# Kernel optimization log

Hardware: AMD Instinct MI355X
Metric: run time of the kernel (lower is better)

## Reference

```python
import jax, jax.numpy as jnp
import numpy as np

EPS = 1e-5
K = 20

def lrelu(x):
    return jnp.where(x >= 0, x, 0.2 * x)

def in2d(x):  # [B,C,N,k] instance norm over (N,k), no affine, biased var
    m = jnp.mean(x, axis=(2, 3), keepdims=True)
    v = jnp.var(x, axis=(2, 3), keepdims=True)
    return (x - m) * jax.lax.rsqrt(v + EPS)

def in1d(x):  # [B,C,N] instance norm over N
    m = jnp.mean(x, axis=2, keepdims=True)
    v = jnp.var(x, axis=2, keepdims=True)
    return (x - m) * jax.lax.rsqrt(v + EPS)

def knn_idx(x, k):  # x: [B,C,N]; uses only first 3 channels (as original)
    p = x[:, :3, :]
    inner = -2.0 * jnp.einsum('bcn,bcm->bnm', p, p)
    xx = jnp.sum(p * p, axis=1)  # [B,N]
    pd = -xx[:, :, None] - inner - xx[:, None, :]  # negative squared dist [B,N,N]
    return jax.lax.top_k(pd, k)[1]  # [B,N,k]

def graph_feature(x, k):  # x: [B,C,N] -> [B,2C,N,k]
    idx = knn_idx(x, k)
    xT = jnp.transpose(x, (0, 2, 1))  # [B,N,C]
    feat = jax.vmap(lambda t, i: t[i])(xT, idx)  # [B,N,k,C]
    center = xT[:, :, None, :]
    out = jnp.concatenate([feat - center, jnp.broadcast_to(center, feat.shape)], axis=3)
    return jnp.transpose(out, (0, 3, 1, 2))  # [B,2C,N,k]

def conv2d1(w, x):  # 1x1 conv2d: w [O,C], x [B,C,N,k]
    return jnp.einsum('oc,bcnk->bonk', w, x)

def conv1d1(w, x):  # 1x1 conv1d: w [O,C], x [B,C,N]
    return jnp.einsum('oc,bcn->bon', w, x)

def setup_inputs() -> dict:
    key = jax.random.key(0)
    ks = jax.random.split(key, 10)
    def w(k, o, c):
        return jax.random.normal(k, (o, c), dtype=jnp.float32) * np.float32(1.0 / np.sqrt(c))
    return {
        'x':  jax.random.normal(ks[0], (4, 4096, 4), dtype=jnp.float32),
        'w1': w(ks[1], 64, 8),
        'w2': w(ks[2], 64, 64),
        'w3': w(ks[3], 64, 128),
        'w4': w(ks[4], 64, 64),
        'w5': w(ks[5], 64, 128),
        'w6': w(ks[6], 1024, 192),
        'w7': w(ks[7], 512, 1216),
        'w8': w(ks[8], 256, 512),
        'w9': w(ks[9], 2, 256),
    }

def reference(x, w1, w2, w3, w4, w5, w6, w7, w8, w9):
    xt = jnp.transpose(x, (0, 2, 1))  # [B,4,N]
    num_points = xt.shape[2]
    # EdgeConv block 1
    f = graph_feature(xt, K)                     # [B,8,N,k]
    h = lrelu(in2d(conv2d1(w1, f)))
    h = lrelu(in2d(conv2d1(w2, h)))
    x1 = jnp.max(h, axis=-1)                     # [B,64,N]
    # EdgeConv block 2
    f = graph_feature(x1, K)                     # [B,128,N,k]
    h = lrelu(in2d(conv2d1(w3, f)))
    h = lrelu(in2d(conv2d1(w4, h)))
    x2 = jnp.max(h, axis=-1)
    # EdgeConv block 3
    f = graph_feature(x2, K)
    h = lrelu(in2d(conv2d1(w5, f)))
    x3 = jnp.max(h, axis=-1)
    # global embedding
    cat = jnp.concatenate([x1, x2, x3], axis=1)  # [B,192,N]
    g = lrelu(in1d(conv1d1(w6, cat)))            # [B,1024,N]
    g = jnp.max(g, axis=-1, keepdims=True)       # [B,1024,1]
    g = jnp.broadcast_to(g, (g.shape[0], g.shape[1], num_points))
    h = jnp.concatenate([g, x1, x2, x3], axis=1) # [B,1216,N]
    h = lrelu(in1d(conv1d1(w7, h)))
    h = lrelu(in1d(conv1d1(w8, h)))
    # dropout identity (eval mode)
    out = conv1d1(w9, h)                         # [B,2,N]
    return jnp.transpose(out, (0, 2, 1))         # [B,N,2]
```

## Files before the change

kernel.cpp:

```cpp
#include <hip/hip_runtime.h>
#include <hip/hip_fp16.h>
#include <math.h>

constexpr int BB  = 4;
constexpr int NN  = 4096;
constexpr int KK  = 20;
constexpr int NKK = NN * KK;
constexpr int TPOS = BB * NKK;
constexpr int NMASK = NN - 1;

#define DEVFN __device__ __forceinline__

DEVFN float lrelu_f(float v) { return v >= 0.f ? v : 0.2f * v; }
DEVFN unsigned fenc(float f) { unsigned u = __float_as_uint(f); return (u & 0x80000000u) ? ~u : (u | 0x80000000u); }

template<int CSTRIDE>
__global__ __launch_bounds__(256) void knn_kernel(const float* __restrict__ xin, int* __restrict__ idxout)
{
    __shared__ float sx[NN], sy[NN], sz[NN];
    __shared__ unsigned shist[256];
    __shared__ unsigned scollv[256];
    __shared__ unsigned long long scoll64[128];
    __shared__ unsigned sres[2];
    __shared__ unsigned scnt[2];
    const int tid = threadIdx.x;
    const int b  = blockIdx.x >> 8;
    const int q0 = (blockIdx.x & 255) * 16;
    for (int i = tid; i < NN; i += 256) {
        const float4 rc = *reinterpret_cast<const float4*>(xin + (size_t)(b*NN + i) * CSTRIDE);
        sx[i] = rc.x; sy[i] = rc.y; sz[i] = rc.z;
    }

    for (int qq = 0; qq < 16; ++qq) {
        __syncthreads();
        shist[tid] = 0;
        if (tid == 0) { scnt[0] = 0; scnt[1] = 0; }
        const int qi = q0 + qq;
        const float qx = sx[qi], qy = sy[qi], qz = sz[qi];
        const float nxx = -__fadd_rn(__fadd_rn(__fmul_rn(qx,qx), __fmul_rn(qy,qy)), __fmul_rn(qz,qz));
        __syncthreads();
        unsigned ukey[NN/256];
#pragma unroll
        for (int i = 0; i < NN/256; ++i) {
            const int m = tid + (i << 8);
            float cx = sx[m], cy = sy[m], cz = sz[m];
            float cw  = __fadd_rn(__fadd_rn(__fmul_rn(cx,cx), __fmul_rn(cy,cy)), __fmul_rn(cz,cz));
            float dot = __fadd_rn(__fadd_rn(__fmul_rn(qx,cx), __fmul_rn(qy,cy)), __fmul_rn(qz,cz));
            float pd  = __fsub_rn(__fsub_rn(nxx, __fmul_rn(-2.f, dot)), cw);
            unsigned u = fenc(pd);
            ukey[i] = u;
            atomicAdd(&shist[u >> 24], 1u);
        }
        __syncthreads();
        if (tid < 64) {
            const int base = 255 - tid*4;
            unsigned h0 = shist[base], h1 = shist[base-1], h2 = shist[base-2], h3 = shist[base-3];
            unsigned s = h0 + h1 + h2 + h3;
            unsigned c = s;
#pragma unroll
            for (int off = 1; off < 64; off <<= 1) { unsigned t = __shfl_up(c, off, 64); if (tid >= off) c += t; }
            unsigned cprev = c - s;
            if (c >= KK && cprev < KK) {
                unsigned cc = cprev; int bb = base;
                if (cc + h0 < KK) { cc += h0; bb = base-1;
                    if (cc + h1 < KK) { cc += h1; bb = base-2;
                        if (cc + h2 < KK) { cc += h2; bb = base-3; } } }
                sres[0] = (unsigned)bb; sres[1] = KK - cc;
            }
        }
        __syncthreads();
        const unsigned b0 = sres[0], K1 = sres[1];
        shist[tid] = 0;
        __syncthreads();
#pragma unroll
        for (int i = 0; i < NN/256; ++i) {
            unsigned u = ukey[i];
            if ((u >> 24) == b0) atomicAdd(&shist[(u >> 16) & 255u], 1u);
        }
        __syncthreads();
        if (tid < 64) {
            const int base = 255 - tid*4;
            unsigned h0 = shist[base], h1 = shist[base-1], h2 = shist[base-2], h3 = shist[base-3];
            unsigned s = h0 + h1 + h2 + h3;
            unsigned c = s;
#pragma unroll
            for (int off = 1; off < 64; off <<= 1) { unsigned t = __shfl_up(c, off, 64); if (tid >= off) c += t; }
            unsigned cprev = c - s;
            if (c >= K1 && cprev < K1) {
                unsigned cc = cprev; int bb = base;
                if (cc + h0 < K1) { cc += h0; bb = base-1;
                    if (cc + h1 < K1) { cc += h1; bb = base-2;
                        if (cc + h2 < K1) { cc += h2; bb = base-3; } } }
                sres[0] = (unsigned)bb; sres[1] = K1 - cc;
            }
        }
        __syncthreads();
        const unsigned prefix16 = (b0 << 8) | sres[0];
        const unsigned K2 = sres[1];
#pragma unroll
        for (int i = 0; i < NN/256; ++i) {
            unsigned u = ukey[i];
            if ((u >> 16) == prefix16) {
                unsigned pos = atomicAdd(&scnt[0], 1u);
                if (pos < 256u) scollv[pos] = u;
            }
        }
        __syncthreads();
        {
            int cb = (int)scnt[0]; if (cb > 256) cb = 256;
            if (tid < cb) {
                unsigned v = scollv[tid];
                unsigned ng = 0, ne = 0;
                for (int j = 0; j < cb; ++j) {
                    unsigned w = scollv[j];
                    ng += (w > v); ne += (w == v);
                }
                if (ng < K2 && ng + ne >= K2) sres[0] = v;
            }
        }
        __syncthreads();
        const unsigned W = sres[0];
#pragma unroll
        for (int i = 0; i < NN/256; ++i) {
            const int m = tid + (i << 8);
            unsigned u = ukey[i];
            if (u >= W) {
                unsigned pos = atomicAdd(&scnt[1], 1u);
                if (pos < 128u) scoll64[pos] = ((unsigned long long)u << 32) | (unsigned)(NN-1 - m);
            }
        }
        __syncthreads();
        {
            int c2 = (int)scnt[1]; if (c2 > 128) c2 = 128;
            if (tid < c2) {
                unsigned long long kv = scoll64[tid];
                int rank = 0;
                for (int j = 0; j < c2; ++j) rank += (scoll64[j] > kv);
                if (rank < KK) {
                    int* op = idxout + ((size_t)(b*NN + qi)) * KK;
                    op[rank] = (NN-1) - (int)(kv & 0xFFFFFFFFull);
                }
            }
        }
    }
}

template<int CINH, int CSTRIDE>
__global__ __launch_bounds__(64) void uv_kernel(const float* __restrict__ xin, const float* __restrict__ w,
                                                float* __restrict__ ub, float* __restrict__ vb)
{
    __shared__ float sp[32][CINH];
    const int lane = threadIdx.x;
    float wa[CINH], wd[CINH];
#pragma unroll
    for (int c = 0; c < CINH; ++c) {
        float a = w[lane*(2*CINH) + c];
        wa[c] = a;
        wd[c] = w[lane*(2*CINH) + CINH + c] - a;
    }
    const int p0 = blockIdx.x * 32;
    for (int i = lane; i < 32*CINH; i += 64) {
        int pi = i / CINH, c = i % CINH;
        sp[pi][c] = xin[(size_t)(p0 + pi)*CSTRIDE + c];
    }
    __syncthreads();
    for (int pi = 0; pi < 32; ++pi) {
        float au = 0.f, av = 0.f;
#pragma unroll
        for (int c = 0; c < CINH; ++c) {
            float xv = sp[pi][c];
            au = fmaf(wa[c], xv, au);
            av = fmaf(wd[c], xv, av);
        }
        ub[(size_t)(p0 + pi)*64 + lane] = au;
        vb[(size_t)(p0 + pi)*64 + lane] = av;
    }
}

template<bool STOREMAX>
__global__ __launch_bounds__(64) void gstat_kernel(const float* __restrict__ ub, const float* __restrict__ vb,
    const int* __restrict__ idx, float* __restrict__ xraw,
    double* __restrict__ ssum, double* __restrict__ ssq)
{
    const int lane = threadIdx.x;
    const int g0 = blockIdx.x * 8;
    const int b = g0 / NN;
    double lsum = 0.0, lsq = 0.0;
    for (int ni = 0; ni < 8; ++ni) {
        const int g = g0 + ni;
        const float v = vb[(size_t)g*64 + lane];
        float vmax = -INFINITY;
        for (int k = 0; k < KK; ++k) {
            const int j = idx[(size_t)g*KK + k] & NMASK;
            float o = ub[(size_t)(b*NN + j)*64 + lane] + v;
            if constexpr (STOREMAX) vmax = fmaxf(vmax, o);
            lsum += (double)o; lsq += (double)o*(double)o;
        }
        if constexpr (STOREMAX) xraw[(size_t)g*64 + lane] = vmax;
    }
    atomicAdd(&ssum[b*64+lane], lsum);
    atomicAdd(&ssq [b*64+lane], lsq);
}

__global__ __launch_bounds__(64) void s1b_kernel(const float* __restrict__ x, const int* __restrict__ idx,
    const float* __restrict__ w1, const float* __restrict__ w2,
    const float* __restrict__ m1, const float* __restrict__ r1,
    float* __restrict__ xraw, double* __restrict__ ssum, double* __restrict__ ssq)
{
    __shared__ float sh[64];
    const int lane = threadIdx.x;
    float wr1[8];
#pragma unroll
    for (int c = 0; c < 8; ++c) wr1[c] = w1[lane*8 + c];
    float wr2[64];
#pragma unroll
    for (int c = 0; c < 64; ++c) wr2[c] = w2[lane*64 + c];
    const int g0 = blockIdx.x * 8;
    const int b = g0 / NN;
    const float mm = m1[b*64+lane], rr = r1[b*64+lane];
    double lsum = 0.0, lsq = 0.0;
    for (int ni = 0; ni < 8; ++ni) {
        const int g = g0 + ni;
        const float4 ct = *reinterpret_cast<const float4*>(x + (size_t)g*4);
        float vmax = -INFINITY;
        for (int k = 0; k < KK; ++k) {
            const int j = idx[(size_t)g*KK + k] & NMASK;
            const float4 nb = *reinterpret_cast<const float4*>(x + (size_t)(b*NN + j)*4);
            float o1 = wr1[0]*(nb.x-ct.x) + wr1[1]*(nb.y-ct.y) + wr1[2]*(nb.z-ct.z) + wr1[3]*(nb.w-ct.w)
                     + wr1[4]*ct.x + wr1[5]*ct.y + wr1[6]*ct.z + wr1[7]*ct.w;
            float h = lrelu_f((o1 - mm) * rr);
            __syncthreads();
            sh[lane] = h;
            __syncthreads();
            float acc = 0.f;
#pragma unroll
            for (int c = 0; c < 64; c += 4) {
                const float4 hv = *reinterpret_cast<const float4*>(&sh[c]);
                acc += wr2[c]*hv.x + wr2[c+1]*hv.y + wr2[c+2]*hv.z + wr2[c+3]*hv.w;
            }
            vmax = fmaxf(vmax, acc);
            lsum += (double)acc; lsq += (double)acc*(double)acc;
        }
        xraw[(size_t)g*64 + lane] = vmax;
    }
    atomicAdd(&ssum[b*64+lane], lsum);
    atomicAdd(&ssq [b*64+lane], lsq);
}

__global__ __launch_bounds__(64) void s2b_kernel(const float* __restrict__ xin, const int* __restrict__ idx,
    const float* __restrict__ w3, const float* __restrict__ w4,
    const float* __restrict__ m3, const float* __restrict__ r3,
    float* __restrict__ xraw, double* __restrict__ ssum, double* __restrict__ ssq)
{
    __shared__ float sf[128];
    __shared__ float sh[64];
    const int lane = threadIdx.x;
    float wr3[128];
#pragma unroll
    for (int c = 0; c < 128; ++c) wr3[c] = w3[lane*128 + c];
    float wr4[64];
#pragma unroll
    for (int c = 0; c < 64; ++c) wr4[c] = w4[lane*64 + c];
    const int g0 = blockIdx.x * 8;
    const int b = g0 / NN;
    const float mm = m3[b*64+lane], rr = r3[b*64+lane];
    double lsum = 0.0, lsq = 0.0;
    for (int ni = 0; ni < 8; ++ni) {
        const int g = g0 + ni;
        const float ctl = xin[(size_t)g*64 + lane];
        float vmax = -INFINITY;
        for (int k = 0; k < KK; ++k) {
            const int j = idx[(size_t)g*KK + k] & NMASK;
            const float nbl = xin[(size_t)(b*NN + j)*64 + lane];
            __syncthreads();
            sf[lane] = nbl - ctl;
            sf[64+lane] = ctl;
            __syncthreads();
            float o3 = 0.f;
#pragma unroll
            for (int c = 0; c < 128; c += 4) {
                const float4 fv = *reinterpret_cast<const float4*>(&sf[c]);
                o3 += wr3[c]*fv.x + wr3[c+1]*fv.y + wr3[c+2]*fv.z + wr3[c+3]*fv.w;
            }
            float h = lrelu_f((o3 - mm) * rr);
            __syncthreads();
            sh[lane] = h;
            __syncthreads();
            float acc = 0.f;
#pragma unroll
            for (int c = 0; c < 64; c += 4) {
                const float4 hv = *reinterpret_cast<const float4*>(&sh[c]);
                acc += wr4[c]*hv.x + wr4[c+1]*hv.y + wr4[c+2]*hv.z + wr4[c+3]*hv.w;
            }
            vmax = fmaxf(vmax, acc);
            lsum += (double)acc; lsq += (double)acc*(double)acc;
        }
        xraw[(size_t)g*64 + lane] = vmax;
    }
    atomicAdd(&ssum[b*64+lane], lsum);
    atomicAdd(&ssq [b*64+lane], lsq);
}

__global__ void fin_kernel(const double* __restrict__ ssum, const double* __restrict__ ssq,
                           float* __restrict__ meanp, float* __restrict__ rstdp, int total, double invn)
{
    int t = blockIdx.x*256 + threadIdx.x;
    if (t >= total) return;
    double m = ssum[t]*invn;
    double v = ssq[t]*invn - m*m;
    meanp[t] = (float)m;
    rstdp[t] = (float)(1.0 / sqrt(v + 1e-5));
}

__global__ void finx_kernel(float* __restrict__ xv, const float* __restrict__ m, const float* __restrict__ r)
{
    int t = blockIdx.x*256 + threadIdx.x;
    int c0 = (t & 15) * 4;
    int b = t >> 16;
    float4 v = *reinterpret_cast<float4*>(xv + (size_t)t*4);
    v.x = lrelu_f((v.x - m[b*64+c0+0]) * r[b*64+c0+0]);
    v.y = lrelu_f((v.y - m[b*64+c0+1]) * r[b*64+c0+1]);
    v.z = lrelu_f((v.z - m[b*64+c0+2]) * r[b*64+c0+2]);
    v.w = lrelu_f((v.w - m[b*64+c0+3]) * r[b*64+c0+3]);
    *reinterpret_cast<float4*>(xv + (size_t)t*4) = v;
}

__global__ void transw_kernel(const float* __restrict__ w, float* __restrict__ wT, int O, int C, int rs, int off)
{
    int t = blockIdx.x*256 + threadIdx.x;
    if (t >= O*C) return;
    int o = t % O, c = t / O;
    wT[t] = w[(size_t)o*rs + off + c];
}

__global__ __launch_bounds__(256) void conv7a_kernel(
    const float* __restrict__ x1, const float* __restrict__ x2, const float* __restrict__ x3,
    const float* __restrict__ wT,
    __half* __restrict__ out7h, double* __restrict__ ssum, double* __restrict__ ssq)
{
    __shared__ float si[32][192];
    const int b = blockIdx.z, nbase = blockIdx.x*32;
    const int o = blockIdx.y*256 + threadIdx.x;
    for (int i = threadIdx.x; i < 32*192; i += 256) {
        int nl = i/192, c = i%192;
        size_t base = (size_t)(b*NN + nbase + nl)*64;
        si[nl][c] = (c < 64) ? x1[base + c] : (c < 128) ? x2[base + c - 64] : x3[base + c - 128];
    }
    __syncthreads();
    float acc[32];
#pragma unroll
    for (int n = 0; n < 32; ++n) acc[n] = 0.f;
    for (int c = 0; c < 192; ++c) {
        float wv = wT[(size_t)c*512 + o];
#pragma unroll
        for (int n = 0; n < 32; ++n) acc[n] = fmaf(wv, si[n][c], acc[n]);
    }
    double ps = 0.0, pq = 0.0;
#pragma unroll
    for (int n = 0; n < 32; ++n) {
        out7h[(size_t)(b*NN + nbase + n)*512 + o] = __float2half(acc[n]);
        ps += (double)acc[n]; pq += (double)acc[n]*(double)acc[n];
    }
    atomicAdd(&ssum[b*512+o], ps);
    atomicAdd(&ssq [b*512+o], pq);
}

__global__ __launch_bounds__(256) void conv8k_kernel(
    const __half* __restrict__ out7h, const float* __restrict__ m7, const float* __restrict__ r7,
    const float* __restrict__ wT8,
    float* __restrict__ out8, double* __restrict__ ssum, double* __restrict__ ssq)
{
    __shared__ float h7[16][512];
    const int b = blockIdx.y, nbase = blockIdx.x*16;
    const int tid = threadIdx.x;
    for (int i = tid; i < 16*512; i += 256) {
        int nl = i >> 9, c = i & 511;
        float v = __half2float(out7h[(size_t)(b*NN + nbase + nl)*512 + c]);
        h7[nl][c] = lrelu_f((v - m7[b*512+c]) * r7[b*512+c]);
    }
    __syncthreads();
    const int o = tid;
    float acc8[16];
#pragma unroll
    for (int n = 0; n < 16; ++n) acc8[n] = 0.f;
    for (int c = 0; c < 512; ++c) {
        float wv = wT8[(size_t)c*256 + o];
#pragma unroll
        for (int n = 0; n < 16; ++n) acc8[n] = fmaf(wv, h7[n][c], acc8[n]);
    }
    double ps = 0.0, pq = 0.0;
#pragma unroll
    for (int n = 0; n < 16; ++n) {
        out8[(size_t)(b*NN + nbase + n)*256 + o] = acc8[n];
        ps += (double)acc8[n]; pq += (double)acc8[n]*(double)acc8[n];
    }
    atomicAdd(&ssum[b*256+o], ps);
    atomicAdd(&ssq [b*256+o], pq);
}

__global__ __launch_bounds__(256) void conv9_kernel(const float* __restrict__ in8,
    const float* __restrict__ meanp, const float* __restrict__ rstdp,
    const float* __restrict__ w9, float* __restrict__ outp)
{
    const int lane = threadIdx.x & 63, wv = threadIdx.x >> 6;
    const int ng = blockIdx.x*4 + wv;
    const int b = ng / NN;
    const int c0 = lane*4;
    const float4 v4 = *reinterpret_cast<const float4*>(&in8[(size_t)ng*256 + c0]);
    float vv[4] = {v4.x, v4.y, v4.z, v4.w};
    float a0 = 0.f, a1 = 0.f;
#pragma unroll
    for (int i = 0; i < 4; ++i) {
        int c = c0 + i;
        float a = lrelu_f((vv[i] - meanp[b*256+c]) * rstdp[b*256+c]);
        a0 = fmaf(w9[c],     a, a0);
        a1 = fmaf(w9[256+c], a, a1);
    }
#pragma unroll
    for (int off = 32; off > 0; off >>= 1) {
        a0 += __shfl_down(a0, off, 64);
        a1 += __shfl_down(a1, off, 64);
    }
    if (lane == 0) { outp[(size_t)ng*2 + 0] = a0; outp[(size_t)ng*2 + 1] = a1; }
}

extern "C" void kernel_launch(void* const* d_in, const int* in_sizes, int n_in,
                              void* d_out, int out_size, void* d_ws, size_t ws_size,
                              hipStream_t stream)
{
    const float* x  = (const float*)d_in[0];
    const float* w1 = (const float*)d_in[1];
    const float* w2 = (const float*)d_in[2];
    const float* w3 = (const float*)d_in[3];
    const float* w4 = (const float*)d_in[4];
    const float* w5 = (const float*)d_in[5];
    const float* w7 = (const float*)d_in[7];
    const float* w8 = (const float*)d_in[8];
    const float* w9 = (const float*)d_in[9];
    float* outp = (float*)d_out;

    char* ws = (char*)d_ws;
    size_t off = 0;
    auto alloc = [&](size_t bytes) -> void* {
        void* p = ws + off;
        off = (off + bytes + 255) & ~(size_t)255;
        return p;
    };
    double* dstats = (double*)alloc((size_t)16896 * 8);
    unsigned* u6max = (unsigned*)alloc((size_t)4096 * 4);
    float* fstats = (float*)alloc((size_t)14848 * 4);
    int*   idxb  = (int*)  alloc((size_t)TPOS * 4);
    float* wT7   = (float*)alloc((size_t)512*192*4);
    float* wT8   = (float*)alloc((size_t)256*512*4);
    char*  sc17  = (char*) alloc((size_t)BB*NN*512*2);
    float* ubuf  = (float*)sc17;
    float* vbuf  = (float*)(sc17 + (size_t)BB*NN*64*4);
    __half* out7h = (__half*)sc17;
    float* x1v   = (float*)alloc((size_t)BB*NN*64*4);
    float* x2v   = (float*)alloc((size_t)BB*NN*64*4);
    float* x3v   = (float*)alloc((size_t)BB*NN*64*4);
    float* out8  = (float*)alloc((size_t)BB*NN*256*4);

    (void)u6max;
    double* d1 = dstats;           double* d2 = dstats + 512;
    double* d3 = dstats + 1024;    double* d4 = dstats + 1536;
    double* d5 = dstats + 2048;
    double* d7sum = dstats + 10752; double* d7sq = d7sum + 2048;
    double* d8sum = dstats + 14848; double* d8sq = d8sum + 1024;
    float* m1 = fstats;        float* r1 = fstats + 256;
    float* m2 = fstats + 512;  float* r2 = fstats + 768;
    float* m3 = fstats + 1024; float* r3 = fstats + 1280;
    float* m4 = fstats + 1536; float* r4 = fstats + 1792;
    float* m5 = fstats + 2048; float* r5 = fstats + 2304;
    float* m7 = fstats + 6656; float* r7 = fstats + 8704;
    float* m8 = fstats + 12800; float* r8 = fstats + 13824;

    hipMemsetAsync(dstats, 0, (size_t)16896*8 + (size_t)4096*4, stream);

    transw_kernel<<<384, 256, 0, stream>>>(w7, wT7, 512, 192, 1216, 1024);
    transw_kernel<<<512, 256, 0, stream>>>(w8, wT8, 256, 512, 512, 0);

    knn_kernel<4><<<1024, 256, 0, stream>>>(x, idxb);
    uv_kernel<4, 4><<<512, 64, 0, stream>>>(x, w1, ubuf, vbuf);
    gstat_kernel<false><<<2048, 64, 0, stream>>>(ubuf, vbuf, idxb, nullptr, d1, d1+256);
    fin_kernel<<<1, 256, 0, stream>>>(d1, d1+256, m1, r1, 256, 1.0/81920.0);
    s1b_kernel<<<2048, 64, 0, stream>>>(x, idxb, w1, w2, m1, r1, x1v, d2, d2+256);
    fin_kernel<<<1, 256, 0, stream>>>(d2, d2+256, m2, r2, 256, 1.0/81920.0);
    finx_kernel<<<1024, 256, 0, stream>>>(x1v, m2, r2);

    knn_kernel<64><<<1024, 256, 0, stream>>>(x1v, idxb);
    uv_kernel<64, 64><<<512, 64, 0, stream>>>(x1v, w3, ubuf, vbuf);
    gstat_kernel<false><<<2048, 64, 0, stream>>>(ubuf, vbuf, idxb, nullptr, d3, d3+256);
    fin_kernel<<<1, 256, 0, stream>>>(d3, d3+256, m3, r3, 256, 1.0/81920.0);
    s2b_kernel<<<2048, 64, 0, stream>>>(x1v, idxb, w3, w4, m3, r3, x2v, d4, d4+256);
    fin_kernel<<<1, 256, 0, stream>>>(d4, d4+256, m4, r4, 256, 1.0/81920.0);
    finx_kernel<<<1024, 256, 0, stream>>>(x2v, m4, r4);

    knn_kernel<64><<<1024, 256, 0, stream>>>(x2v, idxb);
    uv_kernel<64, 64><<<512, 64, 0, stream>>>(x2v, w5, ubuf, vbuf);
    gstat_kernel<true><<<2048, 64, 0, stream>>>(ubuf, vbuf, idxb, x3v, d5, d5+256);
    fin_kernel<<<1, 256, 0, stream>>>(d5, d5+256, m5, r5, 256, 1.0/81920.0);
    finx_kernel<<<1024, 256, 0, stream>>>(x3v, m5, r5);

    conv7a_kernel<<<dim3(128, 2, 4), 256, 0, stream>>>(x1v, x2v, x3v, wT7, out7h, d7sum, d7sq);
    fin_kernel<<<8, 256, 0, stream>>>(d7sum, d7sq, m7, r7, 2048, 1.0/4096.0);
    conv8k_kernel<<<dim3(256, 4), 256, 0, stream>>>(out7h, m7, r7, wT8, out8, d8sum, d8sq);
    fin_kernel<<<4, 256, 0, stream>>>(d8sum, d8sq, m8, r8, 1024, 1.0/4096.0);
    conv9_kernel<<<4096, 256, 0, stream>>>(out8, m8, r8, w9, outp);
}
```

Baseline: 1.559 ms.

## Process two kNN queries per block concurrently and widen gstat to one point per wave

```diff
diff --git a/kernel.cpp b/kernel.cpp
--- a/kernel.cpp
+++ b/kernel.cpp
@@ -18,12 +18,13 @@
 __global__ __launch_bounds__(256) void knn_kernel(const float* __restrict__ xin, int* __restrict__ idxout)
 {
     __shared__ float sx[NN], sy[NN], sz[NN];
-    __shared__ unsigned shist[256];
-    __shared__ unsigned scollv[256];
-    __shared__ unsigned long long scoll64[128];
-    __shared__ unsigned sres[2];
-    __shared__ unsigned scnt[2];
-    const int tid = threadIdx.x;
+    __shared__ unsigned shist[2][256];
+    __shared__ unsigned long long spool64[2][128];
+    __shared__ unsigned sres[2][2];
+    __shared__ unsigned scnt[2][2];
+    const int tid  = threadIdx.x;
+    const int half = tid >> 7;
+    const int t2   = tid & 127;
     const int b  = blockIdx.x >> 8;
     const int q0 = (blockIdx.x & 255) * 16;
     for (int i = tid; i < NN; i += 256) {
@@ -31,109 +32,112 @@
         sx[i] = rc.x; sy[i] = rc.y; sz[i] = rc.z;
     }
 
-    for (int qq = 0; qq < 16; ++qq) {
-        __syncthreads();
-        shist[tid] = 0;
-        if (tid == 0) { scnt[0] = 0; scnt[1] = 0; }
-        const int qi = q0 + qq;
+    unsigned* scollv = reinterpret_cast<unsigned*>(&spool64[half][0]);
+    unsigned long long* scoll64 = &spool64[half][0];
+
+    for (int qq = 0; qq < 8; ++qq) {
+        __syncthreads();
+        shist[half][t2] = 0; shist[half][t2 + 128] = 0;
+        if (t2 == 0) { scnt[half][0] = 0; scnt[half][1] = 0; }
+        const int qi = q0 + qq*2 + half;
         const float qx = sx[qi], qy = sy[qi], qz = sz[qi];
         const float nxx = -__fadd_rn(__fadd_rn(__fmul_rn(qx,qx), __fmul_rn(qy,qy)), __fmul_rn(qz,qz));
         __syncthreads();
-        unsigned ukey[NN/256];
-#pragma unroll
-        for (int i = 0; i < NN/256; ++i) {
-            const int m = tid + (i << 8);
+        unsigned ukey[NN/128];
+#pragma unroll
+        for (int i = 0; i < NN/128; ++i) {
+            const int m = t2 + (i << 7);
             float cx = sx[m], cy = sy[m], cz = sz[m];
             float cw  = __fadd_rn(__fadd_rn(__fmul_rn(cx,cx), __fmul_rn(cy,cy)), __fmul_rn(cz,cz));
             float dot = __fadd_rn(__fadd_rn(__fmul_rn(qx,cx), __fmul_rn(qy,cy)), __fmul_rn(qz,cz));
             float pd  = __fsub_rn(__fsub_rn(nxx, __fmul_rn(-2.f, dot)), cw);
             unsigned u = fenc(pd);
             ukey[i] = u;
-            atomicAdd(&shist[u >> 24], 1u);
-        }
-        __syncthreads();
-        if (tid < 64) {
-            const int base = 255 - tid*4;
-            unsigned h0 = shist[base], h1 = shist[base-1], h2 = shist[base-2], h3 = shist[base-3];
+            atomicAdd(&shist[half][u >> 24], 1u);
+        }
+        __syncthreads();
+        if (t2 < 64) {
+            const int base = 255 - t2*4;
+            unsigned h0 = shist[half][base], h1 = shist[half][base-1], h2 = shist[half][base-2], h3 = shist[half][base-3];
             unsigned s = h0 + h1 + h2 + h3;
             unsigned c = s;
 #pragma unroll
-            for (int off = 1; off < 64; off <<= 1) { unsigned t = __shfl_up(c, off, 64); if (tid >= off) c += t; }
+            for (int off = 1; off < 64; off <<= 1) { unsigned t = __shfl_up(c, off, 64); if (t2 >= off) c += t; }
             unsigned cprev = c - s;
             if (c >= KK && cprev < KK) {
                 unsigned cc = cprev; int bb = base;
                 if (cc + h0 < KK) { cc += h0; bb = base-1;
                     if (cc + h1 < KK) { cc += h1; bb = base-2;
                         if (cc + h2 < KK) { cc += h2; bb = base-3; } } }
-                sres[0] = (unsigned)bb; sres[1] = KK - cc;
-            }
-        }
-        __syncthreads();
-        const unsigned b0 = sres[0], K1 = sres[1];
-        shist[tid] = 0;
-        __syncthreads();
-#pragma unroll
-        for (int i = 0; i < NN/256; ++i) {
+                sres[half][0] = (unsigned)bb; sres[half][1] = KK - cc;
+            }
+        }
+        __syncthreads();
+        const unsigned b0 = sres[half][0], K1 = sres[half][1];
+        shist[half][t2] = 0; shist[half][t2 + 128] = 0;
+        __syncthreads();
+#pragma unroll
+        for (int i = 0; i < NN/128; ++i) {
             unsigned u = ukey[i];
-            if ((u >> 24) == b0) atomicAdd(&shist[(u >> 16) & 255u], 1u);
-        }
-        __syncthreads();
-        if (tid < 64) {
-            const int base = 255 - tid*4;
-            unsigned h0 = shist[base], h1 = shist[base-1], h2 = shist[base-2], h3 = shist[base-3];
+            if ((u >> 24) == b0) atomicAdd(&shist[half][(u >> 16) & 255u], 1u);
+        }
+        __syncthreads();
+        if (t2 < 64) {
+            const int base = 255 - t2*4;
+            unsigned h0 = shist[half][base], h1 = shist[half][base-1], h2 = shist[half][base-2], h3 = shist[half][base-3];
             unsigned s = h0 + h1 + h2 + h3;
             unsigned c = s;
 #pragma unroll
-            for (int off = 1; off < 64; off <<= 1) { unsigned t = __shfl_up(c, off, 64); if (tid >= off) c += t; }
+            for (int off = 1; off < 64; off <<= 1) { unsigned t = __shfl_up(c, off, 64); if (t2 >= off) c += t; }
             unsigned cprev = c - s;
             if (c >= K1 && cprev < K1) {
                 unsigned cc = cprev; int bb = base;
                 if (cc + h0 < K1) { cc += h0; bb = base-1;
                     if (cc + h1 < K1) { cc += h1; bb = base-2;
                         if (cc + h2 < K1) { cc += h2; bb = base-3; } } }
-                sres[0] = (unsigned)bb; sres[1] = K1 - cc;
-            }
-        }
-        __syncthreads();
-        const unsigned prefix16 = (b0 << 8) | sres[0];
-        const unsigned K2 = sres[1];
-#pragma unroll
-        for (int i = 0; i < NN/256; ++i) {
+                sres[half][0] = (unsigned)bb; sres[half][1] = K1 - cc;
+            }
+        }
+        __syncthreads();
+        const unsigned prefix16 = (b0 << 8) | sres[half][0];
+        const unsigned K2 = sres[half][1];
+#pragma unroll
+        for (int i = 0; i < NN/128; ++i) {
             unsigned u = ukey[i];
             if ((u >> 16) == prefix16) {
-                unsigned pos = atomicAdd(&scnt[0], 1u);
+                unsigned pos = atomicAdd(&scnt[half][0], 1u);
                 if (pos < 256u) scollv[pos] = u;
             }
         }
         __syncthreads();
         {
-            int cb = (int)scnt[0]; if (cb > 256) cb = 256;
-            if (tid < cb) {
-                unsigned v = scollv[tid];
+            int cb = (int)scnt[half][0]; if (cb > 256) cb = 256;
+            for (int cand = t2; cand < cb; cand += 128) {
+                unsigned v = scollv[cand];
                 unsigned ng = 0, ne = 0;
                 for (int j = 0; j < cb; ++j) {
                     unsigned w = scollv[j];
                     ng += (w > v); ne += (w == v);
                 }
-                if (ng < K2 && ng + ne >= K2) sres[0] = v;
-            }
-        }
-        __syncthreads();
-        const unsigned W = sres[0];
-#pragma unroll
-        for (int i = 0; i < NN/256; ++i) {
-            const int m = tid + (i << 8);
+                if (ng < K2 && ng + ne >= K2) sres[half][0] = v;
+            }
+        }
+        __syncthreads();
+        const unsigned W = sres[half][0];
+#pragma unroll
+        for (int i = 0; i < NN/128; ++i) {
+            const int m = t2 + (i << 7);
             unsigned u = ukey[i];
             if (u >= W) {
-                unsigned pos = atomicAdd(&scnt[1], 1u);
+                unsigned pos = atomicAdd(&scnt[half][1], 1u);
                 if (pos < 128u) scoll64[pos] = ((unsigned long long)u << 32) | (unsigned)(NN-1 - m);
             }
         }
         __syncthreads();
         {
-            int c2 = (int)scnt[1]; if (c2 > 128) c2 = 128;
-            if (tid < c2) {
-                unsigned long long kv = scoll64[tid];
+            int c2 = (int)scnt[half][1]; if (c2 > 128) c2 = 128;
+            if (t2 < c2) {
+                unsigned long long kv = scoll64[t2];
                 int rank = 0;
                 for (int j = 0; j < c2; ++j) rank += (scoll64[j] > kv);
                 if (rank < KK) {
@@ -178,26 +182,24 @@
 }
 
 template<bool STOREMAX>
-__global__ __launch_bounds__(64) void gstat_kernel(const float* __restrict__ ub, const float* __restrict__ vb,
+__global__ __launch_bounds__(256) void gstat_kernel(const float* __restrict__ ub, const float* __restrict__ vb,
     const int* __restrict__ idx, float* __restrict__ xraw,
     double* __restrict__ ssum, double* __restrict__ ssq)
 {
-    const int lane = threadIdx.x;
-    const int g0 = blockIdx.x * 8;
-    const int b = g0 / NN;
+    const int lane = threadIdx.x & 63;
+    const int wv   = threadIdx.x >> 6;
+    const int g = blockIdx.x * 4 + wv;
+    const int b = g >> 12;
+    const float v = vb[(size_t)g*64 + lane];
     double lsum = 0.0, lsq = 0.0;
-    for (int ni = 0; ni < 8; ++ni) {
-        const int g = g0 + ni;
-        const float v = vb[(size_t)g*64 + lane];
-        float vmax = -INFINITY;
-        for (int k = 0; k < KK; ++k) {
-            const int j = idx[(size_t)g*KK + k] & NMASK;
-            float o = ub[(size_t)(b*NN + j)*64 + lane] + v;
-            if constexpr (STOREMAX) vmax = fmaxf(vmax, o);
-            lsum += (double)o; lsq += (double)o*(double)o;
-        }
-        if constexpr (STOREMAX) xraw[(size_t)g*64 + lane] = vmax;
-    }
+    float vmax = -INFINITY;
+    for (int k = 0; k < KK; ++k) {
+        const int j = idx[(size_t)g*KK + k] & NMASK;
+        float o = ub[(size_t)(b*NN + j)*64 + lane] + v;
+        if constexpr (STOREMAX) vmax = fmaxf(vmax, o);
+        lsum += (double)o; lsq += (double)o*(double)o;
+    }
+    if constexpr (STOREMAX) xraw[(size_t)g*64 + lane] = vmax;
     atomicAdd(&ssum[b*64+lane], lsum);
     atomicAdd(&ssq [b*64+lane], lsq);
 }
@@ -482,7 +484,7 @@
 
     knn_kernel<4><<<1024, 256, 0, stream>>>(x, idxb);
     uv_kernel<4, 4><<<512, 64, 0, stream>>>(x, w1, ubuf, vbuf);
-    gstat_kernel<false><<<2048, 64, 0, stream>>>(ubuf, vbuf, idxb, nullptr, d1, d1+256);
+    gstat_kernel<false><<<4096, 256, 0, stream>>>(ubuf, vbuf, idxb, nullptr, d1, d1+256);
     fin_kernel<<<1, 256, 0, stream>>>(d1, d1+256, m1, r1, 256, 1.0/81920.0);
     s1b_kernel<<<2048, 64, 0, stream>>>(x, idxb, w1, w2, m1, r1, x1v, d2, d2+256);
     fin_kernel<<<1, 256, 0, stream>>>(d2, d2+256, m2, r2, 256, 1.0/81920.0);
@@ -490,7 +492,7 @@
 
     knn_kernel<64><<<1024, 256, 0, stream>>>(x1v, idxb);
     uv_kernel<64, 64><<<512, 64, 0, stream>>>(x1v, w3, ubuf, vbuf);
-    gstat_kernel<false><<<2048, 64, 0, stream>>>(ubuf, vbuf, idxb, nullptr, d3, d3+256);
+    gstat_kernel<false><<<4096, 256, 0, stream>>>(ubuf, vbuf, idxb, nullptr, d3, d3+256);
     fin_kernel<<<1, 256, 0, stream>>>(d3, d3+256, m3, r3, 256, 1.0/81920.0);
     s2b_kernel<<<2048, 64, 0, stream>>>(x1v, idxb, w3, w4, m3, r3, x2v, d4, d4+256);
     fin_kernel<<<1, 256, 0, stream>>>(d4, d4+256, m4, r4, 256, 1.0/81920.0);
@@ -498,7 +500,7 @@
 
     knn_kernel<64><<<1024, 256, 0, stream>>>(x2v, idxb);
     uv_kernel<64, 64><<<512, 64, 0, stream>>>(x2v, w5, ubuf, vbuf);
-    gstat_kernel<true><<<2048, 64, 0, stream>>>(ubuf, vbuf, idxb, x3v, d5, d5+256);
+    gstat_kernel<true><<<4096, 256, 0, stream>>>(ubuf, vbuf, idxb, x3v, d5, d5+256);
     fin_kernel<<<1, 256, 0, stream>>>(d5, d5+256, m5, r5, 256, 1.0/81920.0);
     finx_kernel<<<1024, 256, 0, stream>>>(x3v, m5, r5);
 
```

New measurement: 1.884 ms. +20.8%, slower.
